# Kernel optimization log

Hardware: AMD Instinct MI355X
Metric: run time of the kernel (lower is better)

Reference implementation:

```python
import jax, jax.numpy as jnp
import numpy as np
from jax import lax


def _conv(x, w, b):
    # NCHW valid conv, stride 1 (torch Conv2d semantics)
    y = lax.conv_general_dilated(x, w, (1, 1), 'VALID',
                                 dimension_numbers=('NCHW', 'OIHW', 'NCHW'))
    return y + b[None, :, None, None]


def _maxpool(x, k, s):
    return lax.reduce_window(x, -jnp.inf, lax.max, (1, 1, k, k), (1, 1, s, s), 'VALID')


def _lin(x, w, b):
    # torch nn.Linear: y = x @ W^T + b, applied to last dim
    return x @ w.T + b


def setup_inputs() -> dict:
    key = jax.random.key(0)
    ks = jax.random.split(key, 21)
    def f(i, shape, scale):
        return jax.random.normal(ks[i], shape, dtype=jnp.float32) * scale
    return {
        'x': f(0, (512, 1, 28, 28), 1.0),
        'c1_w': f(1, (50, 1, 3, 3), 0.33), 'c1_b': f(2, (50,), 0.1),
        'c2_w': f(3, (50, 50, 3, 3), 0.047), 'c2_b': f(4, (50,), 0.05),
        'c3_w': f(5, (50, 50, 3, 3), 0.047), 'c3_b': f(6, (50,), 0.05),
        'l1_w': f(7, (500, 50), 0.14), 'l1_b': f(8, (500,), 0.05),
        'l2_w': f(9, (10, 500), 0.045), 'l2_b': f(10, (10,), 0.05),
        'd1_w': f(11, (3, 8450), 0.011), 'd1_b': f(12, (3,), 0.05),
        'd2_w': f(13, (2, 1250), 0.028), 'd2_b': f(14, (2,), 0.05),
        'c1c3_w': f(15, (13, 13), 0.28), 'c1c3_b': f(16, (13,), 0.05),
        'c1l1_w': f(17, (500, 1), 1.0), 'c1l1_b': f(18, (500,), 0.05),
        'c2l1_w': f(19, (500, 5), 0.45), 'c2l1_b': f(20, (500,), 0.05),
    }


def reference(x, c1_w, c1_b, c2_w, c2_b, c3_w, c3_b, l1_w, l1_b, l2_w, l2_b,
              d1_w, d1_b, d2_w, d2_b, c1c3_w, c1c3_b, c1l1_w, c1l1_b,
              c2l1_w, c2l1_b):
    B = x.shape[0]
    # stage 1: conv1 + relu + pool2 -> [B,50,13,13]
    h1 = _maxpool(jax.nn.relu(_conv(x, c1_w, c1_b)), 2, 2)
    # router 1 (argmax over 3 branches): 0 -> conv2 path, 1 -> c1_c3 path, 2 -> early-exit linear path
    d1 = jnp.argmax(_lin(h1.reshape(B, -1), d1_w, d1_b), axis=1)  # [B]
    # branch l11 (d1==2): pool7 -> [B,50,1,1], Linear(1->500) on last dim -> [B,50,1,500]
    l11 = _lin(_maxpool(h1, 7, 7), c1l1_w, c1l1_b)
    # branch c3-direct (d1==1): Linear(13->13) on last dim, then conv3+relu+pool2 -> [B,50,5,5]
    c33 = _lin(h1, c1c3_w, c1c3_b)
    c3d = _maxpool(jax.nn.relu(_conv(c33, c3_w, c3_b)), 2, 2)
    # branch c2 (d1==0): conv2+relu+pool2 -> [B,50,5,5]
    h2 = _maxpool(jax.nn.relu(_conv(h1, c2_w, c2_b)), 2, 2)
    # router 2 (argmax over 2 sub-branches)
    d2 = jnp.argmax(_lin(h2.reshape(B, -1), d2_w, d2_b), axis=1)  # [B]
    # sub-branch c32 (d2==0): conv3+relu+pool2 -> [B,50,1,1]
    c32 = _maxpool(jax.nn.relu(_conv(h2, c3_w, c3_b)), 2, 2)
    # sub-branch l12 (d2==1): Linear(5->500) on last dim -> [B,50,5,500], pool3 -> [B,50,1,166]
    l12 = _maxpool(_lin(h2, c2l1_w, c2l1_b), 3, 3)

    def head(t):
        # original: .view(-1, 50) -> linear1/relu/linear2/log_softmax; row-major flatten per sample
        r = t.reshape(B, -1, 50)
        return jax.nn.log_softmax(_lin(jax.nn.relu(_lin(r, l1_w, l1_b)), l2_w, l2_b), axis=-1)

    dt = x.dtype
    m_l11 = (d1 == 2).astype(dt)[:, None, None]
    m_c3d = (d1 == 1).astype(dt)[:, None, None]
    m_c32 = ((d1 == 0) & (d2 == 0)).astype(dt)[:, None, None]
    m_l12 = ((d1 == 0) & (d2 == 1)).astype(dt)[:, None, None]
    # dense masked combine (static-shape equivalent of the gather/compute/concat dispatch);
    # branch order matches the original concatenation: l11, l12, c32, c3-direct
    out = jnp.concatenate([head(l11) * m_l11, head(l12) * m_l12,
                           head(c32) * m_c32, head(c3d) * m_c3d], axis=1)  # [B,692,10]
    return out, d1, d2
```

## Files before the change

### kernel.cpp

```cpp
#include <hip/hip_runtime.h>
#include <hip/hip_bf16.h>
#include <math.h>

#define BB 512
#define CC 50

typedef __attribute__((ext_vector_type(8))) __bf16 bf16x8;
typedef __attribute__((ext_vector_type(4))) float f32x4;

__global__ void k_zero(float* __restrict__ out, int n4) {
  int i = blockIdx.x * 256 + threadIdx.x;
  if (i < n4) {
    float4 z = {0.f, 0.f, 0.f, 0.f};
    ((float4*)out)[i] = z;
  }
}

__global__ void k_pack(const float* __restrict__ l1w, const float* __restrict__ l1b,
                       const float* __restrict__ l2w,
                       __bf16* __restrict__ W1p, __bf16* __restrict__ W2p) {
  int idx = blockIdx.x * 256 + threadIdx.x;
  if (idx < 512 * 64) {
    int j = idx >> 6, k = idx & 63;
    float v = 0.f;
    if (j < 500) {
      if (k < 50) v = l1w[j * 50 + k];
      else if (k == 50) v = l1b[j];
    }
    W1p[idx] = (__bf16)v;
  } else if (idx < 512 * 64 + 16 * 512) {
    int i2 = idx - 512 * 64;
    int n = i2 >> 9, k2 = i2 & 511;
    float v = (n < 10 && k2 < 500) ? l2w[n * 500 + k2] : 0.f;
    W2p[i2] = (__bf16)v;
  }
}

__global__ void k_conv1(const float* __restrict__ x, const float* __restrict__ w,
                        const float* __restrict__ bias, float* __restrict__ h1) {
  int idx = blockIdx.x * 256 + threadIdx.x;
  if (idx >= BB * CC * 169) return;
  int b = idx / (CC * 169);
  int rem = idx % (CC * 169);
  int c = rem / 169;
  int p = rem % 169;
  int py = p / 13, px = p % 13;
  const float* xi = x + b * 784;
  float wr[9];
#pragma unroll
  for (int i = 0; i < 9; i++) wr[i] = w[c * 9 + i];
  float m = -INFINITY;
#pragma unroll
  for (int dy = 0; dy < 2; dy++)
#pragma unroll
    for (int dx = 0; dx < 2; dx++) {
      int y0 = 2 * py + dy, x0 = 2 * px + dx;
      float s = 0.f;
#pragma unroll
      for (int ky = 0; ky < 3; ky++)
#pragma unroll
        for (int kx = 0; kx < 3; kx++)
          s += xi[(y0 + ky) * 28 + x0 + kx] * wr[ky * 3 + kx];
      m = fmaxf(m, s);
    }
  h1[idx] = fmaxf(m + bias[c], 0.f);
}

__global__ void k_d1(const float* __restrict__ h1, const float* __restrict__ w,
                     const float* __restrict__ bias, int* __restrict__ d1i,
                     float* __restrict__ outd1) {
  int b = blockIdx.x, t = threadIdx.x;
  const float* hb = h1 + b * 8450;
  float s0 = 0.f, s1 = 0.f, s2 = 0.f;
  for (int i = t; i < 8450; i += 256) {
    float v = hb[i];
    s0 += v * w[i];
    s1 += v * w[8450 + i];
    s2 += v * w[16900 + i];
  }
#pragma unroll
  for (int off = 32; off >= 1; off >>= 1) {
    s0 += __shfl_down(s0, off);
    s1 += __shfl_down(s1, off);
    s2 += __shfl_down(s2, off);
  }
  __shared__ float red[4][3];
  if ((t & 63) == 0) { red[t >> 6][0] = s0; red[t >> 6][1] = s1; red[t >> 6][2] = s2; }
  __syncthreads();
  if (t == 0) {
    float l0 = bias[0], l1v = bias[1], l2v = bias[2];
    for (int wv = 0; wv < 4; wv++) { l0 += red[wv][0]; l1v += red[wv][1]; l2v += red[wv][2]; }
    int idx = 0; float best = l0;
    if (l1v > best) { best = l1v; idx = 1; }
    if (l2v > best) { best = l2v; idx = 2; }
    d1i[b] = idx;
    outd1[b] = (float)idx;
  }
}

__global__ void k_d2(const float* __restrict__ h2, const float* __restrict__ w,
                     const float* __restrict__ bias, int* __restrict__ d2i,
                     float* __restrict__ outd2) {
  int b = blockIdx.x, t = threadIdx.x;
  const float* hb = h2 + b * 1250;
  float s0 = 0.f, s1 = 0.f;
  for (int i = t; i < 1250; i += 256) {
    float v = hb[i];
    s0 += v * w[i];
    s1 += v * w[1250 + i];
  }
#pragma unroll
  for (int off = 32; off >= 1; off >>= 1) {
    s0 += __shfl_down(s0, off);
    s1 += __shfl_down(s1, off);
  }
  __shared__ float red[4][2];
  if ((t & 63) == 0) { red[t >> 6][0] = s0; red[t >> 6][1] = s1; }
  __syncthreads();
  if (t == 0) {
    float l0 = bias[0] + red[0][0] + red[1][0] + red[2][0] + red[3][0];
    float l1v = bias[1] + red[0][1] + red[1][1] + red[2][1] + red[3][1];
    int idx = (l1v > l0) ? 1 : 0;
    d2i[b] = idx;
    outd2[b] = (float)idx;
  }
}

__global__ void k_p7(const float* __restrict__ h1, float* __restrict__ p7) {
  int idx = blockIdx.x * 256 + threadIdx.x;
  if (idx >= BB * CC) return;
  int b = idx / CC, c = idx % CC;
  const float* hp = h1 + b * 8450 + c * 169;
  float m = -INFINITY;
#pragma unroll
  for (int y = 0; y < 7; y++)
#pragma unroll
    for (int x = 0; x < 7; x++) m = fmaxf(m, hp[y * 13 + x]);
  p7[idx] = m;
}

template <int MODE>
__global__ __launch_bounds__(256) void k_conv5(const float* __restrict__ in,
                                               const float* __restrict__ w,
                                               const float* __restrict__ bias,
                                               const int* __restrict__ d1i,
                                               float* __restrict__ out) {
  int b = blockIdx.x;
  if (MODE == 1 && d1i[b] != 1) return;
  __shared__ float sh[8450];
  for (int i = threadIdx.x; i < 8450; i += 256) sh[i] = in[b * 8450 + i];
  __syncthreads();
  int t = threadIdx.x;
  if (t >= 250) return;
  int oc = t / 5, py = t % 5;
  float acc[5][4];
#pragma unroll
  for (int i = 0; i < 5; i++)
#pragma unroll
    for (int j = 0; j < 4; j++) acc[i][j] = 0.f;
  const float* wb = w + oc * 450;
  for (int ic = 0; ic < 50; ic++) {
    float wv[9];
#pragma unroll
    for (int i = 0; i < 9; i++) wv[i] = wb[ic * 9 + i];
    float r[4][13];
    const float* rp = sh + ic * 169 + 2 * py * 13;
#pragma unroll
    for (int rr = 0; rr < 4; rr++)
#pragma unroll
      for (int cx = 0; cx < 13; cx++) r[rr][cx] = rp[rr * 13 + cx];
#pragma unroll
    for (int px = 0; px < 5; px++)
#pragma unroll
      for (int dy = 0; dy < 2; dy++)
#pragma unroll
        for (int dx = 0; dx < 2; dx++) {
          float s = acc[px][dy * 2 + dx];
          int x0 = 2 * px + dx;
#pragma unroll
          for (int ky = 0; ky < 3; ky++)
#pragma unroll
            for (int kx = 0; kx < 3; kx++)
              s += r[dy + ky][x0 + kx] * wv[ky * 3 + kx];
          acc[px][dy * 2 + dx] = s;
        }
  }
  float bs = bias[oc];
#pragma unroll
  for (int px = 0; px < 5; px++) {
    float m = fmaxf(fmaxf(acc[px][0], acc[px][1]), fmaxf(acc[px][2], acc[px][3]));
    out[((b * 50 + oc) * 5 + py) * 5 + px] = fmaxf(m + bs, 0.f);
  }
}

__global__ void k_c33(float* __restrict__ h1, const float* __restrict__ w,
                      const float* __restrict__ bias, const int* __restrict__ d1i) {
  int idx = blockIdx.x * 256 + threadIdx.x;
  if (idx >= BB * CC * 13) return;
  int b = idx / (CC * 13);
  if (d1i[b] != 1) return;
  float* row = h1 + b * 8450 + (idx % (CC * 13)) * 13;
  float r[13];
#pragma unroll
  for (int k = 0; k < 13; k++) r[k] = row[k];
#pragma unroll
  for (int x = 0; x < 13; x++) {
    float s = bias[x];
    const float* wx = w + x * 13;
#pragma unroll
    for (int k = 0; k < 13; k++) s += r[k] * wx[k];
    row[x] = s;
  }
}

__global__ void k_c32k(const float* __restrict__ h2, const float* __restrict__ w,
                       const float* __restrict__ bias, const int* __restrict__ d1i,
                       const int* __restrict__ d2i, float* __restrict__ c32) {
  int idx = blockIdx.x * 256 + threadIdx.x;
  if (idx >= BB * CC) return;
  int b = idx / CC, oc = idx % CC;
  if (d1i[b] != 0 || d2i[b] != 0) return;
  const float* hb = h2 + b * 1250;
  const float* wb = w + oc * 450;
  float a[4] = {0.f, 0.f, 0.f, 0.f};
  for (int ic = 0; ic < 50; ic++) {
    float r[4][4];
#pragma unroll
    for (int y = 0; y < 4; y++)
#pragma unroll
      for (int x = 0; x < 4; x++) r[y][x] = hb[ic * 25 + y * 5 + x];
    float wv[9];
#pragma unroll
    for (int i = 0; i < 9; i++) wv[i] = wb[ic * 9 + i];
#pragma unroll
    for (int py = 0; py < 2; py++)
#pragma unroll
      for (int px = 0; px < 2; px++) {
        float s = a[py * 2 + px];
#pragma unroll
        for (int ky = 0; ky < 3; ky++)
#pragma unroll
          for (int kx = 0; kx < 3; kx++)
            s += r[py + ky][px + kx] * wv[ky * 3 + kx];
        a[py * 2 + px] = s;
      }
  }
  float m = fmaxf(fmaxf(a[0], a[1]), fmaxf(a[2], a[3]));
  c32[idx] = fmaxf(m + bias[oc], 0.f);
}

__global__ __launch_bounds__(256) void k_l12(const float* __restrict__ h2,
                                             const float* __restrict__ c2l1w,
                                             const float* __restrict__ c2l1b,
                                             const int* __restrict__ d1i,
                                             const int* __restrict__ d2i,
                                             float* __restrict__ l12) {
  int b = blockIdx.x;
  if (d1i[b] != 0 || d2i[b] != 1) return;
  __shared__ float wls[2500];
  __shared__ float bls[500];
  __shared__ float hs[1250];
  int t = threadIdx.x;
  for (int i = t; i < 2500; i += 256) wls[i] = c2l1w[i];
  for (int i = t; i < 500; i += 256) bls[i] = c2l1b[i];
  for (int i = t; i < 1250; i += 256) hs[i] = h2[b * 1250 + i];
  __syncthreads();
  for (int o = t; o < 8300; o += 256) {
    int c = o / 166, tt = o % 166;
    const float* hb = hs + c * 25;
    float m = -INFINITY;
#pragma unroll
    for (int i = 0; i < 3; i++) {
      float a0 = hb[i * 5 + 0], a1 = hb[i * 5 + 1], a2 = hb[i * 5 + 2],
            a3 = hb[i * 5 + 3], a4 = hb[i * 5 + 4];
#pragma unroll
      for (int dj = 0; dj < 3; dj++) {
        int j = 3 * tt + dj;
        const float* wj = wls + j * 5;
        float s = bls[j] + a0 * wj[0] + a1 * wj[1] + a2 * wj[2] + a3 * wj[3] + a4 * wj[4];
        m = fmaxf(m, s);
      }
    }
    l12[b * 8300 + o] = m;
  }
}

__global__ __launch_bounds__(256) void k_head(
    const float* __restrict__ h2, const float* __restrict__ c3d,
    const float* __restrict__ c32, const float* __restrict__ p7,
    const float* __restrict__ l12buf,
    const int* __restrict__ d1i, const int* __restrict__ d2i,
    const __bf16* __restrict__ W1p, const __bf16* __restrict__ W2p,
    const float* __restrict__ l2b,
    const float* __restrict__ c1l1w, const float* __restrict__ c1l1b,
    float* __restrict__ out) {
  int b = blockIdx.x >> 1;
  int half = blockIdx.x & 1;
  int d1 = d1i[b], d2 = d2i[b];
  int branch, nrows, rstart;
  if (d1 == 2)      { branch = 0; nrows = 500; rstart = 0; }
  else if (d1 == 1) { branch = 3; nrows = 25;  rstart = 667; }
  else if (d2 == 1) { branch = 1; nrows = 166; rstart = 500; }
  else              { branch = 2; nrows = 1;   rstart = 666; }
  int base = half * 256;
  if (base >= nrows) return;
  int nr = nrows - base; if (nr > 256) nr = 256;

  __shared__ __align__(16) char smem[256 * 72 * 2];
  __bf16* Vs = (__bf16*)smem;
  __bf16* Ht = (__bf16*)smem;
  int t = threadIdx.x;

  for (int idx = t; idx < 256 * 64; idx += 256) {
    int row = idx >> 6, col = idx & 63;
    float val = 0.f;
    if (col == 50) val = 1.0f;
    else if (col < 50 && row < nr) {
      int rr = base + row;
      if (branch == 0) {
        int c = rr / 10; int j = (rr % 10) * 50 + col;
        val = p7[b * 50 + c] * c1l1w[j] + c1l1b[j];
      } else if (branch == 1) {
        val = l12buf[b * 8300 + rr * 50 + col];
      } else if (branch == 2) {
        val = c32[b * 50 + col];
      } else {
        int k = rr * 50 + col; int c = k / 25, s5 = k % 25;
        val = c3d[(b * 50 + c) * 25 + s5];
      }
    }
    Vs[row * 72 + col] = (__bf16)val;
  }
  __syncthreads();

  int wv = t >> 6, lane = t & 63;
  int lr = lane & 15, lg = lane >> 4;
  int wbase = wv * 64;
  bool active = wbase < nr;
  int wrem = active ? (nr - wbase) : 0;
  int nmt = (wrem + 15) >> 4; if (nmt > 4) nmt = 4;

  bf16x8 a1[4][2];
  if (active) {
#pragma unroll
    for (int mt = 0; mt < 4; ++mt) {
      if (mt < nmt) {
#pragma unroll
        for (int ks = 0; ks < 2; ++ks)
          a1[mt][ks] = *(const bf16x8*)(Vs + (wbase + mt * 16 + lr) * 72 + ks * 32 + lg * 8);
      }
    }
  }
  __syncthreads();
  if (!active) return;

  const __bf16* w1b = W1p + lr * 64 + lg * 8;
  const __bf16* w2b = W2p + lr * 512 + lg * 8;
  f32x4 acc2[4];
#pragma unroll
  for (int mt = 0; mt < 4; ++mt) acc2[mt] = (f32x4){0.f, 0.f, 0.f, 0.f};

  bf16x8 pA0 = *(const bf16x8*)(w1b);
  bf16x8 pA1 = *(const bf16x8*)(w1b + 32);
  bf16x8 pB0 = *(const bf16x8*)(w1b + 1024);
  bf16x8 pB1 = *(const bf16x8*)(w1b + 1024 + 32);
  bf16x8 b2n = *(const bf16x8*)(w2b);

  for (int q = 0; q < 16; ++q) {
    {
      bf16x8 b0 = pA0, b1 = pA1;
      if (q < 15) {
        pA0 = *(const bf16x8*)(w1b + (2 * q + 2) * 1024);
        pA1 = *(const bf16x8*)(w1b + (2 * q + 2) * 1024 + 32);
      }
#pragma unroll
      for (int mt = 0; mt < 4; ++mt) {
        if (mt < nmt) {
          f32x4 dz = {0.f, 0.f, 0.f, 0.f};
          f32x4 d = __builtin_amdgcn_mfma_f32_16x16x32_bf16(a1[mt][0], b0, dz, 0, 0, 0);
          d = __builtin_amdgcn_mfma_f32_16x16x32_bf16(a1[mt][1], b1, d, 0, 0, 0);
          __bf16* hp = Ht + (wv * 4 + mt) * 640;
#pragma unroll
          for (int r = 0; r < 4; ++r)
            hp[(lg * 4 + r) * 40 + lr] = (__bf16)fmaxf(d[r], 0.f);
        }
      }
    }
    {
      bf16x8 b0 = pB0, b1 = pB1;
      if (q < 15) {
        pB0 = *(const bf16x8*)(w1b + (2 * q + 3) * 1024);
        pB1 = *(const bf16x8*)(w1b + (2 * q + 3) * 1024 + 32);
      }
#pragma unroll
      for (int mt = 0; mt < 4; ++mt) {
        if (mt < nmt) {
          f32x4 dz = {0.f, 0.f, 0.f, 0.f};
          f32x4 d = __builtin_amdgcn_mfma_f32_16x16x32_bf16(a1[mt][0], b0, dz, 0, 0, 0);
          d = __builtin_amdgcn_mfma_f32_16x16x32_bf16(a1[mt][1], b1, d, 0, 0, 0);
          __bf16* hp = Ht + (wv * 4 + mt) * 640;
#pragma unroll
          for (int r = 0; r < 4; ++r)
            hp[(lg * 4 + r) * 40 + 16 + lr] = (__bf16)fmaxf(d[r], 0.f);
        }
      }
    }
    {
      bf16x8 bb2 = b2n;
      if (q < 15) b2n = *(const bf16x8*)(w2b + (q + 1) * 32);
#pragma unroll
      for (int mt = 0; mt < 4; ++mt) {
        if (mt < nmt) {
          bf16x8 a2 = *(const bf16x8*)(Ht + (wv * 4 + mt) * 640 + lr * 40 + lg * 8);
          acc2[mt] = __builtin_amdgcn_mfma_f32_16x16x32_bf16(a2, bb2, acc2[mt], 0, 0, 0);
        }
      }
    }
  }

  float bl = (lr < 10) ? l2b[lr] : 0.f;
#pragma unroll
  for (int mt = 0; mt < 4; ++mt) {
    if (mt < nmt) {
      float o[4], m[4], s[4];
#pragma unroll
      for (int r = 0; r < 4; ++r) {
        o[r] = acc2[mt][r] + bl;
        m[r] = (lr < 10) ? o[r] : -INFINITY;
      }
#pragma unroll
      for (int mk = 1; mk < 16; mk <<= 1)
#pragma unroll
        for (int r = 0; r < 4; ++r) m[r] = fmaxf(m[r], __shfl_xor(m[r], mk));
#pragma unroll
      for (int r = 0; r < 4; ++r) s[r] = (lr < 10) ? expf(o[r] - m[r]) : 0.f;
#pragma unroll
      for (int mk = 1; mk < 16; mk <<= 1)
#pragma unroll
        for (int r = 0; r < 4; ++r) s[r] += __shfl_xor(s[r], mk);
      if (lr < 10) {
#pragma unroll
        for (int r = 0; r < 4; ++r) {
          int rloc = wbase + mt * 16 + lg * 4 + r;
          if (rloc < nr)
            out[(b * 692 + rstart + base + rloc) * 10 + lr] = o[r] - (m[r] + logf(s[r]));
        }
      }
    }
  }
}

extern "C" void kernel_launch(void* const* d_in, const int* in_sizes, int n_in,
                              void* d_out, int out_size, void* d_ws, size_t ws_size,
                              hipStream_t stream) {
  const float* x     = (const float*)d_in[0];
  const float* c1w   = (const float*)d_in[1];
  const float* c1b   = (const float*)d_in[2];
  const float* c2w   = (const float*)d_in[3];
  const float* c2b   = (const float*)d_in[4];
  const float* c3w   = (const float*)d_in[5];
  const float* c3b   = (const float*)d_in[6];
  const float* l1w   = (const float*)d_in[7];
  const float* l1b   = (const float*)d_in[8];
  const float* l2w   = (const float*)d_in[9];
  const float* l2b   = (const float*)d_in[10];
  const float* d1w   = (const float*)d_in[11];
  const float* d1b   = (const float*)d_in[12];
  const float* d2w   = (const float*)d_in[13];
  const float* d2b   = (const float*)d_in[14];
  const float* c13w  = (const float*)d_in[15];
  const float* c13b  = (const float*)d_in[16];
  const float* c1l1w = (const float*)d_in[17];
  const float* c1l1b = (const float*)d_in[18];
  const float* c2l1w = (const float*)d_in[19];
  const float* c2l1b = (const float*)d_in[20];
  float* out = (float*)d_out;

  float* ws  = (float*)d_ws;
  float* h1  = ws;
  float* h2  = h1 + 4326400;
  float* c3d = h2 + 640000;
  float* c32 = c3d + 640000;
  float* p7  = c32 + 25600;
  int*   d1i = (int*)(p7 + 25600);
  int*   d2i = d1i + 512;
  __bf16* W1p = (__bf16*)(d2i + 512);
  __bf16* W2p = W1p + 512 * 64;
  float* l12buf = h1;

  float* outd1 = out + 512 * 692 * 10;
  float* outd2 = outd1 + 512;

  k_zero<<<3460, 256, 0, stream>>>(out, 885510);
  k_pack<<<160, 256, 0, stream>>>(l1w, l1b, l2w, W1p, W2p);
  k_conv1<<<16900, 256, 0, stream>>>(x, c1w, c1b, h1);
  k_d1<<<512, 256, 0, stream>>>(h1, d1w, d1b, d1i, outd1);
  k_p7<<<100, 256, 0, stream>>>(h1, p7);
  k_conv5<0><<<512, 256, 0, stream>>>(h1, c2w, c2b, d1i, h2);
  k_d2<<<512, 256, 0, stream>>>(h2, d2w, d2b, d2i, outd2);
  k_c33<<<1300, 256, 0, stream>>>(h1, c13w, c13b, d1i);
  k_conv5<1><<<512, 256, 0, stream>>>(h1, c3w, c3b, d1i, c3d);
  k_c32k<<<100, 256, 0, stream>>>(h2, c3w, c3b, d1i, d2i, c32);
  k_l12<<<512, 256, 0, stream>>>(h2, c2l1w, c2l1b, d1i, d2i, l12buf);
  k_head<<<1024, 256, 0, stream>>>(h2, c3d, c32, p7, l12buf, d1i, d2i,
                                   W1p, W2p, l2b, c1l1w, c1l1b, out);
}
```

Measured before the change: 253.6 us.

## Fuse router, pooling and branch kernels; stage head weights in swizzled LDS

```diff
diff --git a/kernel.cpp b/kernel.cpp
--- a/kernel.cpp
+++ b/kernel.cpp
@@ -66,9 +66,9 @@
   h1[idx] = fmaxf(m + bias[c], 0.f);
 }
 
-__global__ void k_d1(const float* __restrict__ h1, const float* __restrict__ w,
-                     const float* __restrict__ bias, int* __restrict__ d1i,
-                     float* __restrict__ outd1) {
+__global__ void k_d1p7(const float* __restrict__ h1, const float* __restrict__ w,
+                       const float* __restrict__ bias, int* __restrict__ d1i,
+                       float* __restrict__ outd1, float* __restrict__ p7) {
   int b = blockIdx.x, t = threadIdx.x;
   const float* hb = h1 + b * 8450;
   float s0 = 0.f, s1 = 0.f, s2 = 0.f;
@@ -96,47 +96,15 @@
     d1i[b] = idx;
     outd1[b] = (float)idx;
   }
-}
-
-__global__ void k_d2(const float* __restrict__ h2, const float* __restrict__ w,
-                     const float* __restrict__ bias, int* __restrict__ d2i,
-                     float* __restrict__ outd2) {
-  int b = blockIdx.x, t = threadIdx.x;
-  const float* hb = h2 + b * 1250;
-  float s0 = 0.f, s1 = 0.f;
-  for (int i = t; i < 1250; i += 256) {
-    float v = hb[i];
-    s0 += v * w[i];
-    s1 += v * w[1250 + i];
-  }
-#pragma unroll
-  for (int off = 32; off >= 1; off >>= 1) {
-    s0 += __shfl_down(s0, off);
-    s1 += __shfl_down(s1, off);
-  }
-  __shared__ float red[4][2];
-  if ((t & 63) == 0) { red[t >> 6][0] = s0; red[t >> 6][1] = s1; }
-  __syncthreads();
-  if (t == 0) {
-    float l0 = bias[0] + red[0][0] + red[1][0] + red[2][0] + red[3][0];
-    float l1v = bias[1] + red[0][1] + red[1][1] + red[2][1] + red[3][1];
-    int idx = (l1v > l0) ? 1 : 0;
-    d2i[b] = idx;
-    outd2[b] = (float)idx;
-  }
-}
-
-__global__ void k_p7(const float* __restrict__ h1, float* __restrict__ p7) {
-  int idx = blockIdx.x * 256 + threadIdx.x;
-  if (idx >= BB * CC) return;
-  int b = idx / CC, c = idx % CC;
-  const float* hp = h1 + b * 8450 + c * 169;
-  float m = -INFINITY;
-#pragma unroll
-  for (int y = 0; y < 7; y++)
-#pragma unroll
-    for (int x = 0; x < 7; x++) m = fmaxf(m, hp[y * 13 + x]);
-  p7[idx] = m;
+  if (t < 50) {
+    const float* hp = hb + t * 169;
+    float m = -INFINITY;
+#pragma unroll
+    for (int y = 0; y < 7; y++)
+#pragma unroll
+      for (int x = 0; x < 7; x++) m = fmaxf(m, hp[y * 13 + x]);
+    p7[b * 50 + t] = m;
+  }
 }
 
 template <int MODE>
@@ -144,13 +112,39 @@
                                                const float* __restrict__ w,
                                                const float* __restrict__ bias,
                                                const int* __restrict__ d1i,
+                                               const float* __restrict__ w13,
+                                               const float* __restrict__ b13,
                                                float* __restrict__ out) {
   int b = blockIdx.x;
   if (MODE == 1 && d1i[b] != 1) return;
-  __shared__ float sh[8450];
-  for (int i = threadIdx.x; i < 8450; i += 256) sh[i] = in[b * 8450 + i];
-  __syncthreads();
+  __shared__ float sh[50 * 260];
+  __shared__ float w13s[182];
   int t = threadIdx.x;
+  for (int i = t; i < 8450; i += 256) {
+    int ic = i / 169, r = i % 169;
+    int row = r / 13, xx = r % 13;
+    sh[ic * 260 + row * 20 + xx] = in[b * 8450 + i];
+  }
+  if (MODE == 1) {
+    for (int i = t; i < 182; i += 256) w13s[i] = (i < 169) ? w13[i] : b13[i - 169];
+  }
+  __syncthreads();
+  if (MODE == 1) {
+    for (int p = t; p < 650; p += 256) {
+      float* row = sh + (p / 13) * 260 + (p % 13) * 20;
+      float r[13];
+#pragma unroll
+      for (int k = 0; k < 13; k++) r[k] = row[k];
+#pragma unroll
+      for (int xx = 0; xx < 13; xx++) {
+        float s = w13s[169 + xx];
+#pragma unroll
+        for (int k = 0; k < 13; k++) s += r[k] * w13s[xx * 13 + k];
+        row[xx] = s;
+      }
+    }
+    __syncthreads();
+  }
   if (t >= 250) return;
   int oc = t / 5, py = t % 5;
   float acc[5][4];
@@ -164,11 +158,18 @@
 #pragma unroll
     for (int i = 0; i < 9; i++) wv[i] = wb[ic * 9 + i];
     float r[4][13];
-    const float* rp = sh + ic * 169 + 2 * py * 13;
-#pragma unroll
-    for (int rr = 0; rr < 4; rr++)
-#pragma unroll
-      for (int cx = 0; cx < 13; cx++) r[rr][cx] = rp[rr * 13 + cx];
+    const float* rp = sh + ic * 260 + 2 * py * 20;
+#pragma unroll
+    for (int rr = 0; rr < 4; rr++) {
+      const float* p4 = rp + rr * 20;
+      float4 q0 = *(const float4*)(p4);
+      float4 q1 = *(const float4*)(p4 + 4);
+      float4 q2 = *(const float4*)(p4 + 8);
+      r[rr][0] = q0.x; r[rr][1] = q0.y; r[rr][2] = q0.z; r[rr][3] = q0.w;
+      r[rr][4] = q1.x; r[rr][5] = q1.y; r[rr][6] = q1.z; r[rr][7] = q1.w;
+      r[rr][8] = q2.x; r[rr][9] = q2.y; r[rr][10] = q2.z; r[rr][11] = q2.w;
+      r[rr][12] = p4[12];
+    }
 #pragma unroll
     for (int px = 0; px < 5; px++)
 #pragma unroll
@@ -193,96 +194,106 @@
   }
 }
 
-__global__ void k_c33(float* __restrict__ h1, const float* __restrict__ w,
-                      const float* __restrict__ bias, const int* __restrict__ d1i) {
-  int idx = blockIdx.x * 256 + threadIdx.x;
-  if (idx >= BB * CC * 13) return;
-  int b = idx / (CC * 13);
-  if (d1i[b] != 1) return;
-  float* row = h1 + b * 8450 + (idx % (CC * 13)) * 13;
-  float r[13];
-#pragma unroll
-  for (int k = 0; k < 13; k++) r[k] = row[k];
-#pragma unroll
-  for (int x = 0; x < 13; x++) {
-    float s = bias[x];
-    const float* wx = w + x * 13;
-#pragma unroll
-    for (int k = 0; k < 13; k++) s += r[k] * wx[k];
-    row[x] = s;
-  }
-}
-
-__global__ void k_c32k(const float* __restrict__ h2, const float* __restrict__ w,
-                       const float* __restrict__ bias, const int* __restrict__ d1i,
-                       const int* __restrict__ d2i, float* __restrict__ c32) {
-  int idx = blockIdx.x * 256 + threadIdx.x;
-  if (idx >= BB * CC) return;
-  int b = idx / CC, oc = idx % CC;
-  if (d1i[b] != 0 || d2i[b] != 0) return;
-  const float* hb = h2 + b * 1250;
-  const float* wb = w + oc * 450;
-  float a[4] = {0.f, 0.f, 0.f, 0.f};
-  for (int ic = 0; ic < 50; ic++) {
-    float r[4][4];
-#pragma unroll
-    for (int y = 0; y < 4; y++)
-#pragma unroll
-      for (int x = 0; x < 4; x++) r[y][x] = hb[ic * 25 + y * 5 + x];
-    float wv[9];
-#pragma unroll
-    for (int i = 0; i < 9; i++) wv[i] = wb[ic * 9 + i];
-#pragma unroll
-    for (int py = 0; py < 2; py++)
-#pragma unroll
-      for (int px = 0; px < 2; px++) {
-        float s = a[py * 2 + px];
-#pragma unroll
-        for (int ky = 0; ky < 3; ky++)
-#pragma unroll
-          for (int kx = 0; kx < 3; kx++)
-            s += r[py + ky][px + kx] * wv[ky * 3 + kx];
-        a[py * 2 + px] = s;
-      }
-  }
-  float m = fmaxf(fmaxf(a[0], a[1]), fmaxf(a[2], a[3]));
-  c32[idx] = fmaxf(m + bias[oc], 0.f);
-}
-
-__global__ __launch_bounds__(256) void k_l12(const float* __restrict__ h2,
+__global__ __launch_bounds__(256) void k_d2c(const float* __restrict__ h2,
+                                             const float* __restrict__ d2w,
+                                             const float* __restrict__ d2b,
+                                             const float* __restrict__ c3w,
+                                             const float* __restrict__ c3b,
                                              const float* __restrict__ c2l1w,
                                              const float* __restrict__ c2l1b,
                                              const int* __restrict__ d1i,
-                                             const int* __restrict__ d2i,
+                                             int* __restrict__ d2i,
+                                             float* __restrict__ outd2,
+                                             float* __restrict__ c32,
                                              float* __restrict__ l12) {
-  int b = blockIdx.x;
-  if (d1i[b] != 0 || d2i[b] != 1) return;
+  int b = blockIdx.x, t = threadIdx.x;
+  __shared__ float hs[1250];
   __shared__ float wls[2500];
   __shared__ float bls[500];
-  __shared__ float hs[1250];
-  int t = threadIdx.x;
-  for (int i = t; i < 2500; i += 256) wls[i] = c2l1w[i];
-  for (int i = t; i < 500; i += 256) bls[i] = c2l1b[i];
+  __shared__ float red[4][2];
+  __shared__ int sd2;
   for (int i = t; i < 1250; i += 256) hs[i] = h2[b * 1250 + i];
   __syncthreads();
-  for (int o = t; o < 8300; o += 256) {
-    int c = o / 166, tt = o % 166;
-    const float* hb = hs + c * 25;
-    float m = -INFINITY;
-#pragma unroll
-    for (int i = 0; i < 3; i++) {
-      float a0 = hb[i * 5 + 0], a1 = hb[i * 5 + 1], a2 = hb[i * 5 + 2],
-            a3 = hb[i * 5 + 3], a4 = hb[i * 5 + 4];
-#pragma unroll
-      for (int dj = 0; dj < 3; dj++) {
-        int j = 3 * tt + dj;
-        const float* wj = wls + j * 5;
-        float s = bls[j] + a0 * wj[0] + a1 * wj[1] + a2 * wj[2] + a3 * wj[3] + a4 * wj[4];
-        m = fmaxf(m, s);
-      }
-    }
-    l12[b * 8300 + o] = m;
-  }
+  float s0 = 0.f, s1 = 0.f;
+  for (int i = t; i < 1250; i += 256) {
+    float v = hs[i];
+    s0 += v * d2w[i];
+    s1 += v * d2w[1250 + i];
+  }
+#pragma unroll
+  for (int off = 32; off >= 1; off >>= 1) {
+    s0 += __shfl_down(s0, off);
+    s1 += __shfl_down(s1, off);
+  }
+  if ((t & 63) == 0) { red[t >> 6][0] = s0; red[t >> 6][1] = s1; }
+  __syncthreads();
+  if (t == 0) {
+    float l0 = d2b[0] + red[0][0] + red[1][0] + red[2][0] + red[3][0];
+    float l1v = d2b[1] + red[0][1] + red[1][1] + red[2][1] + red[3][1];
+    int idx = (l1v > l0) ? 1 : 0;
+    d2i[b] = idx;
+    outd2[b] = (float)idx;
+    sd2 = idx;
+  }
+  __syncthreads();
+  int d2v = sd2;
+  if (d1i[b] != 0) return;
+  if (d2v == 0) {
+    if (t < 50) {
+      const float* wb = c3w + t * 450;
+      float a[4] = {0.f, 0.f, 0.f, 0.f};
+      for (int ic = 0; ic < 50; ic++) {
+        float r[4][4];
+#pragma unroll
+        for (int y = 0; y < 4; y++)
+#pragma unroll
+          for (int xx = 0; xx < 4; xx++) r[y][xx] = hs[ic * 25 + y * 5 + xx];
+        float wv[9];
+#pragma unroll
+        for (int i = 0; i < 9; i++) wv[i] = wb[ic * 9 + i];
+#pragma unroll
+        for (int py = 0; py < 2; py++)
+#pragma unroll
+          for (int px = 0; px < 2; px++) {
+            float s = a[py * 2 + px];
+#pragma unroll
+            for (int ky = 0; ky < 3; ky++)
+#pragma unroll
+              for (int kx = 0; kx < 3; kx++)
+                s += r[py + ky][px + kx] * wv[ky * 3 + kx];
+            a[py * 2 + px] = s;
+          }
+      }
+      float m = fmaxf(fmaxf(a[0], a[1]), fmaxf(a[2], a[3]));
+      c32[b * 50 + t] = fmaxf(m + c3b[t], 0.f);
+    }
+  } else {
+    for (int i = t; i < 2500; i += 256) wls[i] = c2l1w[i];
+    for (int i = t; i < 500; i += 256) bls[i] = c2l1b[i];
+    __syncthreads();
+    for (int o = t; o < 8300; o += 256) {
+      int c = o / 166, tt = o % 166;
+      const float* hb = hs + c * 25;
+      float m = -INFINITY;
+#pragma unroll
+      for (int i = 0; i < 3; i++) {
+        float a0 = hb[i * 5 + 0], a1 = hb[i * 5 + 1], a2 = hb[i * 5 + 2],
+              a3 = hb[i * 5 + 3], a4 = hb[i * 5 + 4];
+#pragma unroll
+        for (int dj = 0; dj < 3; dj++) {
+          int j = 3 * tt + dj;
+          const float* wj = wls + j * 5;
+          float s = bls[j] + a0 * wj[0] + a1 * wj[1] + a2 * wj[2] + a3 * wj[3] + a4 * wj[4];
+          m = fmaxf(m, s);
+        }
+      }
+      l12[b * 8300 + o] = m;
+    }
+  }
+}
+
+__device__ __forceinline__ int swz(int byteoff) {
+  return byteoff ^ (((byteoff >> 7) & 7) << 4);
 }
 
 __global__ __launch_bounds__(256) void k_head(
@@ -306,9 +317,10 @@
   if (base >= nrows) return;
   int nr = nrows - base; if (nr > 256) nr = 256;
 
-  __shared__ __align__(16) char smem[256 * 72 * 2];
+  __shared__ __align__(16) char smem[53248];
   __bf16* Vs = (__bf16*)smem;
-  __bf16* Ht = (__bf16*)smem;
+  char* Wst = smem;
+  __bf16* Ht = (__bf16*)(smem + 32768);
   int t = threadIdx.x;
 
   for (int idx = t; idx < 256 * 64; idx += 256) {
@@ -331,6 +343,13 @@
     }
     Vs[row * 72 + col] = (__bf16)val;
   }
+
+  bf16x8 st[4];
+  {
+    const __bf16* s0 = W1p + t * 32;
+#pragma unroll
+    for (int i = 0; i < 4; ++i) st[i] = *(const bf16x8*)(s0 + i * 8);
+  }
   __syncthreads();
 
   int wv = t >> 6, lane = t & 63;
@@ -352,71 +371,82 @@
     }
   }
   __syncthreads();
-  if (!active) return;
-
-  const __bf16* w1b = W1p + lr * 64 + lg * 8;
+
+  {
+#pragma unroll
+    for (int i = 0; i < 4; ++i)
+      *(bf16x8*)(Wst + swz(t * 64 + i * 16)) = st[i];
+  }
+  __syncthreads();
+
   const __bf16* w2b = W2p + lr * 512 + lg * 8;
   f32x4 acc2[4];
 #pragma unroll
   for (int mt = 0; mt < 4; ++mt) acc2[mt] = (f32x4){0.f, 0.f, 0.f, 0.f};
-
-  bf16x8 pA0 = *(const bf16x8*)(w1b);
-  bf16x8 pA1 = *(const bf16x8*)(w1b + 32);
-  bf16x8 pB0 = *(const bf16x8*)(w1b + 1024);
-  bf16x8 pB1 = *(const bf16x8*)(w1b + 1024 + 32);
   bf16x8 b2n = *(const bf16x8*)(w2b);
 
-  for (int q = 0; q < 16; ++q) {
-    {
-      bf16x8 b0 = pA0, b1 = pA1;
-      if (q < 15) {
-        pA0 = *(const bf16x8*)(w1b + (2 * q + 2) * 1024);
-        pA1 = *(const bf16x8*)(w1b + (2 * q + 2) * 1024 + 32);
-      }
-#pragma unroll
-      for (int mt = 0; mt < 4; ++mt) {
-        if (mt < nmt) {
-          f32x4 dz = {0.f, 0.f, 0.f, 0.f};
-          f32x4 d = __builtin_amdgcn_mfma_f32_16x16x32_bf16(a1[mt][0], b0, dz, 0, 0, 0);
-          d = __builtin_amdgcn_mfma_f32_16x16x32_bf16(a1[mt][1], b1, d, 0, 0, 0);
-          __bf16* hp = Ht + (wv * 4 + mt) * 640;
-#pragma unroll
-          for (int r = 0; r < 4; ++r)
-            hp[(lg * 4 + r) * 40 + lr] = (__bf16)fmaxf(d[r], 0.f);
+  for (int c = 0; c < 4; ++c) {
+    if (c < 3) {
+      const __bf16* s2 = W1p + (c + 1) * 8192 + t * 32;
+#pragma unroll
+      for (int i = 0; i < 4; ++i) st[i] = *(const bf16x8*)(s2 + i * 8);
+    }
+    char* wb = Wst + (c & 1) * 16384;
+    if (active) {
+#pragma unroll
+      for (int ql = 0; ql < 4; ++ql) {
+        int q = c * 4 + ql;
+        int boff = ql * 4096 + lr * 128 + lg * 16;
+        bf16x8 bA0 = *(const bf16x8*)(wb + swz(boff));
+        bf16x8 bA1 = *(const bf16x8*)(wb + swz(boff + 64));
+        bf16x8 bB0 = *(const bf16x8*)(wb + swz(boff + 2048));
+        bf16x8 bB1 = *(const bf16x8*)(wb + swz(boff + 2048 + 64));
+#pragma unroll
+        for (int mt = 0; mt < 4; ++mt) {
+          if (mt < nmt) {
+            f32x4 dz = {0.f, 0.f, 0.f, 0.f};
+            f32x4 d = __builtin_amdgcn_mfma_f32_16x16x32_bf16(a1[mt][0], bA0, dz, 0, 0, 0);
+            d = __builtin_amdgcn_mfma_f32_16x16x32_bf16(a1[mt][1], bA1, d, 0, 0, 0);
+            __bf16* hp = Ht + (wv * 4 + mt) * 640;
+#pragma unroll
+            for (int r = 0; r < 4; ++r)
+              hp[(lg * 4 + r) * 40 + lr] = (__bf16)fmaxf(d[r], 0.f);
+          }
         }
-      }
-    }
-    {
-      bf16x8 b0 = pB0, b1 = pB1;
-      if (q < 15) {
-        pB0 = *(const bf16x8*)(w1b + (2 * q + 3) * 1024);
-        pB1 = *(const bf16x8*)(w1b + (2 * q + 3) * 1024 + 32);
-      }
-#pragma unroll
-      for (int mt = 0; mt < 4; ++mt) {
-        if (mt < nmt) {
-          f32x4 dz = {0.f, 0.f, 0.f, 0.f};
-          f32x4 d = __builtin_amdgcn_mfma_f32_16x16x32_bf16(a1[mt][0], b0, dz, 0, 0, 0);
-          d = __builtin_amdgcn_mfma_f32_16x16x32_bf16(a1[mt][1], b1, d, 0, 0, 0);
-          __bf16* hp = Ht + (wv * 4 + mt) * 640;
-#pragma unroll
-          for (int r = 0; r < 4; ++r)
-            hp[(lg * 4 + r) * 40 + 16 + lr] = (__bf16)fmaxf(d[r], 0.f);
+#pragma unroll
+        for (int mt = 0; mt < 4; ++mt) {
+          if (mt < nmt) {
+            f32x4 dz = {0.f, 0.f, 0.f, 0.f};
+            f32x4 d = __builtin_amdgcn_mfma_f32_16x16x32_bf16(a1[mt][0], bB0, dz, 0, 0, 0);
+            d = __builtin_amdgcn_mfma_f32_16x16x32_bf16(a1[mt][1], bB1, d, 0, 0, 0);
+            __bf16* hp = Ht + (wv * 4 + mt) * 640;
+#pragma unroll
+            for (int r = 0; r < 4; ++r)
+              hp[(lg * 4 + r) * 40 + 16 + lr] = (__bf16)fmaxf(d[r], 0.f);
+          }
         }
-      }
-    }
-    {
-      bf16x8 bb2 = b2n;
-      if (q < 15) b2n = *(const bf16x8*)(w2b + (q + 1) * 32);
-#pragma unroll
-      for (int mt = 0; mt < 4; ++mt) {
-        if (mt < nmt) {
-          bf16x8 a2 = *(const bf16x8*)(Ht + (wv * 4 + mt) * 640 + lr * 40 + lg * 8);
-          acc2[mt] = __builtin_amdgcn_mfma_f32_16x16x32_bf16(a2, bb2, acc2[mt], 0, 0, 0);
+        {
+          bf16x8 bb2 = b2n;
+          if (q < 15) b2n = *(const bf16x8*)(w2b + (q + 1) * 32);
+#pragma unroll
+          for (int mt = 0; mt < 4; ++mt) {
+            if (mt < nmt) {
+              bf16x8 a2 = *(const bf16x8*)(Ht + (wv * 4 + mt) * 640 + lr * 40 + lg * 8);
+              acc2[mt] = __builtin_amdgcn_mfma_f32_16x16x32_bf16(a2, bb2, acc2[mt], 0, 0, 0);
+            }
+          }
         }
       }
     }
-  }
+    if (c < 3) {
+      char* wd = Wst + (1 - (c & 1)) * 16384;
+#pragma unroll
+      for (int i = 0; i < 4; ++i)
+        *(bf16x8*)(wd + swz(t * 64 + i * 16)) = st[i];
+    }
+    __syncthreads();
+  }
+  if (!active) return;
 
   float bl = (lr < 10) ? l2b[lr] : 0.f;
 #pragma unroll
@@ -494,14 +524,11 @@
   k_zero<<<3460, 256, 0, stream>>>(out, 885510);
   k_pack<<<160, 256, 0, stream>>>(l1w, l1b, l2w, W1p, W2p);
   k_conv1<<<16900, 256, 0, stream>>>(x, c1w, c1b, h1);
-  k_d1<<<512, 256, 0, stream>>>(h1, d1w, d1b, d1i, outd1);
-  k_p7<<<100, 256, 0, stream>>>(h1, p7);
-  k_conv5<0><<<512, 256, 0, stream>>>(h1, c2w, c2b, d1i, h2);
-  k_d2<<<512, 256, 0, stream>>>(h2, d2w, d2b, d2i, outd2);
-  k_c33<<<1300, 256, 0, stream>>>(h1, c13w, c13b, d1i);
-  k_conv5<1><<<512, 256, 0, stream>>>(h1, c3w, c3b, d1i, c3d);
-  k_c32k<<<100, 256, 0, stream>>>(h2, c3w, c3b, d1i, d2i, c32);
-  k_l12<<<512, 256, 0, stream>>>(h2, c2l1w, c2l1b, d1i, d2i, l12buf);
+  k_d1p7<<<512, 256, 0, stream>>>(h1, d1w, d1b, d1i, outd1, p7);
+  k_conv5<0><<<512, 256, 0, stream>>>(h1, c2w, c2b, d1i, c13w, c13b, h2);
+  k_conv5<1><<<512, 256, 0, stream>>>(h1, c3w, c3b, d1i, c13w, c13b, c3d);
+  k_d2c<<<512, 256, 0, stream>>>(h2, d2w, d2b, c3w, c3b, c2l1w, c2l1b,
+                                 d1i, d2i, outd2, c32, l12buf);
   k_head<<<1024, 256, 0, stream>>>(h2, c3d, c32, p7, l12buf, d1i, d2i,
                                    W1p, W2p, l2b, c1l1w, c1l1b, out);
 }
```

New measurement: 237.2 us. 1.07x faster.
